# Kernel tuning notes

Hardware: AMD Instinct MI355X
Metric: run time of the kernel (lower is better)

The kernel has to match this reference:

```python
import jax, jax.numpy as jnp
import numpy as np
from jax import lax

N = 100000      # nodes
E = 1600000     # edges
T = 8           # timesteps
DS, DT = 10, 20 # static / temporal features
GH = 64         # gnn_hidden
LH = 64         # lstm_hidden
EC = 64         # end_channels
OC = 1          # out_channels
EPS = 1e-5


def setup_inputs() -> dict:
    key = jax.random.key(0)
    ks = jax.random.split(key, 20)
    g = lambda i, shape, s=0.05: jax.random.normal(ks[i], shape, jnp.float32) * s
    return {
        "x": jax.random.normal(ks[0], (N, DS + DT, T), jnp.float32),
        "edge_index": jax.random.randint(ks[1], (2, E), 0, N, jnp.int64),
        # static encoder (computed in forward but unused downstream, kept for faithfulness)
        "W_static": g(2, (GH, DS)), "b_static": g(3, (GH,)),
        # LSTMCell: input_size = DT + GH, hidden = LH; gate order i,f,g,o
        "W_ih": g(4, (4 * LH, DT + GH)), "W_hh": g(5, (4 * LH, LH)),
        "b_ih": g(6, (4 * LH,)), "b_hh": g(7, (4 * LH,)),
        # GraphConv(lstm_hidden -> gnn_hidden): lin_rel (with bias) on aggregated msgs + lin_root (no bias)
        "W_rel": g(8, (GH, LH)), "b_rel": g(9, (GH,)), "W_root": g(10, (GH, LH)),
        # BatchNorm1d(GH+LH)
        "gamma": jnp.ones((GH + LH,), jnp.float32), "beta": jnp.zeros((GH + LH,), jnp.float32),
        # head: linear1(128->EC), linear2(EC->128), output_layer(128->OC)
        "W1": g(11, (EC, GH + LH)), "b1": g(12, (EC,)),
        "W2": g(13, (GH + LH, EC)), "b2": g(14, (GH + LH,)),
        "W_out": g(15, (OC, GH + LH)), "b_out": g(16, (OC,)),
    }


def reference(x, edge_index, W_static, b_static, W_ih, W_hh, b_ih, b_hh,
              W_rel, b_rel, W_root, gamma, beta, W1, b1, W2, b2, W_out, b_out):
    src, dst = edge_index[0], edge_index[1]
    x_static = x[:, :DS, 0]                      # [N, DS]
    x_temporal = x[:, DS:DS + DT, :]             # [N, DT, T]
    static_embed = x_static @ W_static.T + b_static  # computed but unused (matches source)

    xt_seq = jnp.transpose(x_temporal, (2, 0, 1))  # [T, N, DT]
    h0 = jnp.zeros((N, GH), jnp.float32)
    c0 = jnp.zeros((N, GH), jnp.float32)

    def step(carry, x_t):
        h, c = carry
        # GraphConv: sum-aggregate neighbor h, then linear (linear commutes with sum)
        agg = jax.ops.segment_sum(h[src], dst, num_segments=N)   # [N, LH]
        gnn_out = agg @ W_rel.T + b_rel + h @ W_root.T           # [N, GH]
        inp = jnp.concatenate([x_t, gnn_out], axis=1)            # [N, DT+GH]
        gates = inp @ W_ih.T + b_ih + h @ W_hh.T + b_hh          # [N, 4*LH]
        i, f, g_, o = jnp.split(gates, 4, axis=1)
        c_new = jax.nn.sigmoid(f) * c + jax.nn.sigmoid(i) * jnp.tanh(g_)
        h_new = jax.nn.sigmoid(o) * jnp.tanh(c_new)
        return (h_new, c_new), gnn_out

    (h, c), gnn_outs = lax.scan(step, (h0, c0), xt_seq)
    gnn_out = gnn_outs[-1]  # gnn output computed at the last timestep (pre-update h)

    fused = jnp.concatenate([h, gnn_out], axis=1)                # [N, GH+LH]
    # BatchNorm1d, training-mode batch statistics (dropout p set to 0)
    mean = fused.mean(axis=0)
    var = fused.var(axis=0)
    normed = (fused - mean) * lax.rsqrt(var + EPS) * gamma + beta
    h1 = jax.nn.relu(normed @ W1.T + b1)
    hidden = jax.nn.relu(h1 @ W2.T + b2)
    out = jax.nn.sigmoid(hidden @ W_out.T + b_out)               # binary task -> sigmoid
    return out
```

## Files before the change

### kernel.cpp

```cpp
#include <hip/hip_runtime.h>

#define NN 100000
#define NE 1600000
#define TT 8
#define KF 160
#define XSTR 24
#define HISTB 6250
#define NRANGE 8
#define RSPAN 12500

typedef __attribute__((ext_vector_type(8))) short bf16x8;
typedef __attribute__((ext_vector_type(4))) float f32x4;
typedef unsigned int uint_;
typedef unsigned short ushort_;

__device__ __forceinline__ float sigf(float x) { return 1.f / (1.f + __expf(-x)); }
__device__ __forceinline__ float tanhf_(float x) { return 1.f - 2.f / (__expf(2.f * x) + 1.f); }
__device__ __forceinline__ ushort_ f2b(float f) {
    uint_ u = __float_as_uint(f);
    u += 0x7fff + ((u >> 16) & 1);
    return (ushort_)(u >> 16);
}
__device__ __forceinline__ float bl(uint_ u) { return __uint_as_float(u << 16); }
__device__ __forceinline__ float bh(uint_ u) { return __uint_as_float(u & 0xffff0000u); }
__device__ __forceinline__ void acc8(float* a, uint4 v) {
    a[0] += bl(v.x); a[1] += bh(v.x); a[2] += bl(v.y); a[3] += bh(v.y);
    a[4] += bl(v.z); a[5] += bh(v.z); a[6] += bl(v.w); a[7] += bh(v.w);
}
__device__ __forceinline__ uint_ pk(float a, float b) {
    return (uint_)f2b(a) | ((uint_)f2b(b) << 16);
}

__global__ void k_detect(const int* __restrict__ ei, int* flag) {
    int i = blockIdx.x * 256 + threadIdx.x;
    if (ei[2 * i + 1] != 0) atomicOr(flag, 1);
}

__global__ void k_hist_xt(const int* __restrict__ ei, const int* __restrict__ flag, int* cnt,
                          const float* __restrict__ x, ushort_* __restrict__ xT) {
    int b = blockIdx.x;
    if (b < HISTB) {
        int e = b * 256 + threadIdx.x;
        if (e >= NE) return;
        int is32 = *flag;
        int d = is32 ? ei[NE + e] : ei[2 * (NE + e)];
        atomicAdd(&cnt[d], 1);
    } else {
        if (!xT) return;
        int i = (b - HISTB) * 256 + threadIdx.x;
        if (i >= NN * XSTR) return;
        int n = i / XSTR, kk = i - n * XSTR;
        if (kk < 20) {
            const float* xp = x + (size_t)n * 240 + (10 + kk) * 8;
#pragma unroll
            for (int t = 0; t < 8; t++) xT[(size_t)t * NN * XSTR + i] = f2b(xp[t]);
        } else {
#pragma unroll
            for (int t = 0; t < 8; t++) xT[(size_t)t * NN * XSTR + i] = 0;
        }
    }
}

__global__ void k_scanblk(const int* __restrict__ cnt, int* off, int* bsum) {
    __shared__ int tmp[1024];
    int i = blockIdx.x * 1024 + threadIdx.x;
    int v = (i < NN) ? cnt[i] : 0;
    tmp[threadIdx.x] = v;
    __syncthreads();
    for (int d = 1; d < 1024; d <<= 1) {
        int t = (threadIdx.x >= d) ? tmp[threadIdx.x - d] : 0;
        __syncthreads();
        tmp[threadIdx.x] += t;
        __syncthreads();
    }
    if (i < NN) off[i + 1] = tmp[threadIdx.x];
    if (threadIdx.x == 1023) bsum[blockIdx.x] = tmp[1023];
}

__global__ void k_scantop(int* bsum, int nb) {
    if (threadIdx.x == 0) {
        int run = 0;
        for (int b = 0; b < nb; b++) { int t = bsum[b]; bsum[b] = run; run += t; }
    }
}

__global__ void k_scanadd(int* off, const int* __restrict__ bsum) {
    int i = blockIdx.x * 1024 + threadIdx.x;
    if (i < NN) off[i + 1] += bsum[blockIdx.x];
    if (i == 0) off[0] = 0;
}

__global__ void k_scatter(const int* __restrict__ ei, const int* __restrict__ flag,
                          int* cursor, int* csr) {
    int b = blockIdx.x;
    int range = b & (NRANGE - 1), chunk = b >> 3;
    int e = chunk * 256 + threadIdx.x;
    if (e >= NE) return;
    int is32 = *flag;
    int d = is32 ? ei[NE + e] : ei[2 * (NE + e)];
    if (d / RSPAN != range) return;
    int s = is32 ? ei[e] : ei[2 * e];
    int pos = atomicAdd(&cursor[d], 1);
    csr[pos] = s;
}

__global__ void k_prep(const float* __restrict__ W_ih, const float* __restrict__ W_hh,
                       const float* __restrict__ b_ih, const float* __restrict__ b_hh,
                       const float* __restrict__ W_rel, const float* __restrict__ b_rel,
                       const float* __restrict__ W_root, ushort_* WgB, float* bgp) {
    int n = threadIdx.x;
    int k = blockIdx.x;
    if (k < KF) {
        float v = 0.f;
        if (n < 256) {
            int w = n >> 6, g = (n >> 4) & 3, j = w * 16 + (n & 15);
            int row = g * 64 + j;
            if (k < 20) {
                v = W_ih[row * 84 + k];
            } else if (k >= 24 && k < 88) {
                int kk = k - 24;
                float a = 0.f;
                for (int m = 0; m < 64; m++) a += W_ih[row * 84 + 20 + m] * W_rel[m * 64 + kk];
                v = a;
            } else if (k >= 88 && k < 152) {
                int kk = k - 88;
                float a = W_hh[row * 64 + kk];
                for (int m = 0; m < 64; m++) a += W_ih[row * 84 + 20 + m] * W_root[m * 64 + kk];
                v = a;
            }
        } else {
            int j = n - 256;
            if (k >= 24 && k < 88) v = W_rel[j * 64 + (k - 24)];
            else if (k >= 88 && k < 152) v = W_root[j * 64 + (k - 88)];
        }
        WgB[(size_t)n * KF + k] = f2b(v);
    } else {
        if (n < 256) {
            int j = n >> 2, g = n & 3;
            int row = g * 64 + j;
            float a = b_ih[row] + b_hh[row];
            for (int m = 0; m < 64; m++) a += W_ih[row * 84 + 20 + m] * b_rel[m];
            bgp[n] = a;
        } else {
            bgp[n] = b_rel[n - 256];
        }
    }
}

template <bool LAST>
__device__ __forceinline__ void step_body(const float* __restrict__ x,
                                          const ushort_* __restrict__ xT,
                                          const int* __restrict__ off,
                                          const int* __restrict__ csr,
                                          const ushort_* __restrict__ hbR,
                                          ushort_* __restrict__ hbW,
                                          float* __restrict__ hf,
                                          float* __restrict__ c,
                                          const ushort_* __restrict__ WgB,
                                          const float* __restrict__ bgp,
                                          float* __restrict__ gnn,
                                          float* __restrict__ sums,
                                          float* __restrict__ sumsq, int t) {
    constexpr int NT = LAST ? 5 : 4;
    __shared__ __align__(16) ushort_ Zs[64 * 168];
    const int tid = threadIdx.x;
    const int nblk = blockIdx.x * 64;
    const int w = tid >> 6, lane = tid & 63;
    const int q = lane >> 4, l16 = lane & 15;

#pragma unroll
    for (int i = 0; i < 3; ++i) {
        int slot = tid + 256 * i;
        int n = slot / 12, oo = slot - n * 12;
        int n_g = nblk + n;
        uint4 z = make_uint4(0, 0, 0, 0);
        if (n_g < NN) {
            if (oo < 3) {
                if (xT) {
                    z = *(const uint4*)(xT + ((size_t)t * NN + n_g) * XSTR + oo * 8);
                } else {
                    const float* xp = x + (size_t)n_g * 240 + 80 + (size_t)oo * 64 + t;
                    uint_ r[4];
#pragma unroll
                    for (int p = 0; p < 4; p++) {
                        int k0 = oo * 8 + p * 2;
                        ushort_ b0 = (k0 < 20) ? f2b(xp[p * 16]) : (ushort_)0;
                        ushort_ b1 = (k0 + 1 < 20) ? f2b(xp[p * 16 + 8]) : (ushort_)0;
                        r[p] = (uint_)b0 | ((uint_)b1 << 16);
                    }
                    z = make_uint4(r[0], r[1], r[2], r[3]);
                }
            } else if (oo < 11) {
                z = *(const uint4*)(hbR + (size_t)n_g * 64 + (oo - 3) * 8);
            }
        }
        int oct = (oo < 3) ? oo : ((oo < 11) ? (oo + 8) : 19);
        *(uint4*)(Zs + n * 168 + oct * 8) = z;
    }

    {
        int slot = tid >> 3;
        int l8 = tid & 7;
        for (int nn = slot; nn < 64; nn += 32) {
            int node = nblk + nn;
            float a[8];
#pragma unroll
            for (int i = 0; i < 8; i++) a[i] = 0.f;
            if (t > 0 && node < NN) {
                int e0 = off[node], e1 = off[node + 1];
                int e = e0;
                for (; e + 8 <= e1; e += 8) {
                    uint4 v0 = *(const uint4*)(hbR + (size_t)csr[e] * 64 + l8 * 8);
                    uint4 v1 = *(const uint4*)(hbR + (size_t)csr[e + 1] * 64 + l8 * 8);
                    uint4 v2 = *(const uint4*)(hbR + (size_t)csr[e + 2] * 64 + l8 * 8);
                    uint4 v3 = *(const uint4*)(hbR + (size_t)csr[e + 3] * 64 + l8 * 8);
                    uint4 v4 = *(const uint4*)(hbR + (size_t)csr[e + 4] * 64 + l8 * 8);
                    uint4 v5 = *(const uint4*)(hbR + (size_t)csr[e + 5] * 64 + l8 * 8);
                    uint4 v6 = *(const uint4*)(hbR + (size_t)csr[e + 6] * 64 + l8 * 8);
                    uint4 v7 = *(const uint4*)(hbR + (size_t)csr[e + 7] * 64 + l8 * 8);
                    acc8(a, v0); acc8(a, v1); acc8(a, v2); acc8(a, v3);
                    acc8(a, v4); acc8(a, v5); acc8(a, v6); acc8(a, v7);
                }
                for (; e < e1; e++) {
                    uint4 v0 = *(const uint4*)(hbR + (size_t)csr[e] * 64 + l8 * 8);
                    acc8(a, v0);
                }
            }
            uint4 o;
            o.x = pk(a[0], a[1]); o.y = pk(a[2], a[3]);
            o.z = pk(a[4], a[5]); o.w = pk(a[6], a[7]);
            *(uint4*)(Zs + nn * 168 + 24 + l8 * 8) = o;
        }
    }
    __syncthreads();

    f32x4 acc[4][NT];
#pragma unroll
    for (int mt = 0; mt < 4; mt++)
#pragma unroll
        for (int nt = 0; nt < NT; nt++) acc[mt][nt] = (f32x4)(0.f);

#pragma unroll
    for (int kt = 0; kt < 5; ++kt) {
        bf16x8 af[4], bf[NT];
#pragma unroll
        for (int mt = 0; mt < 4; mt++)
            af[mt] = *(const bf16x8*)(Zs + (mt * 16 + l16) * 168 + kt * 32 + q * 8);
#pragma unroll
        for (int nt = 0; nt < NT; nt++) {
            int n = (nt < 4) ? (w * 64 + nt * 16 + l16) : (256 + w * 16 + l16);
            bf[nt] = *(const bf16x8*)(WgB + (size_t)n * KF + kt * 32 + q * 8);
        }
#pragma unroll
        for (int mt = 0; mt < 4; mt++)
#pragma unroll
            for (int nt = 0; nt < NT; nt++)
                acc[mt][nt] = __builtin_amdgcn_mfma_f32_16x16x32_bf16(af[mt], bf[nt], acc[mt][nt], 0, 0, 0);
    }

    const int j = w * 16 + l16;
    const f32x4 bias = *(const f32x4*)(bgp + j * 4);
    const float brl = LAST ? bgp[256 + j] : 0.f;
    float sh = 0.f, sh2 = 0.f, sg = 0.f, sg2 = 0.f;

    __syncthreads();
    ushort_* Hs   = Zs;
    float*   CsLo = (float*)(Zs + 4096);

    float cnHi[8];
#pragma unroll
    for (int mt = 0; mt < 4; ++mt) {
#pragma unroll
        for (int r = 0; r < 4; ++r) {
            int nloc = mt * 16 + q * 4 + r;
            int node = nblk + nloc;
            float cn = 0.f, hn = 0.f;
            if (node < NN) {
                size_t idx = (size_t)node * 64 + j;
                float iv = sigf(acc[mt][0][r] + bias.x);
                float fv = sigf(acc[mt][1][r] + bias.y);
                float gv = tanhf_(acc[mt][2][r] + bias.z);
                float ov = sigf(acc[mt][3][r] + bias.w);
                cn = fv * c[idx] + iv * gv;
                hn = ov * tanhf_(cn);
                if (LAST) {
                    float gn = acc[mt][4][r] + brl;
                    hf[idx] = hn;
                    gnn[idx] = gn;
                    sh += hn; sh2 += hn * hn;
                    sg += gn; sg2 += gn * gn;
                }
            }
            Hs[nloc * 64 + j] = f2b(hn);
            if (mt < 2) CsLo[nloc * 64 + j] = cn;
            else        cnHi[(mt - 2) * 4 + r] = cn;
        }
    }
    __syncthreads();
#pragma unroll
    for (int i = 0; i < 2; ++i) {
        int s = tid + 256 * i;
        {
            int n = s >> 3, part = s & 7;
            if (nblk + n < NN)
                *(uint4*)(hbW + (size_t)(nblk + n) * 64 + part * 8) =
                    *(const uint4*)(Hs + n * 64 + part * 8);
        }
        {
            int n = s >> 4, part = s & 15;
            if (nblk + n < NN)
                *(float4*)(c + (size_t)(nblk + n) * 64 + part * 4) =
                    *(const float4*)(CsLo + n * 64 + part * 4);
        }
    }
    __syncthreads();
    float* CsHi = (float*)Zs;
#pragma unroll
    for (int mt = 2; mt < 4; ++mt)
#pragma unroll
        for (int r = 0; r < 4; ++r) {
            int nloc = mt * 16 + q * 4 + r;
            CsHi[(nloc - 32) * 64 + j] = cnHi[(mt - 2) * 4 + r];
        }
    __syncthreads();
#pragma unroll
    for (int i = 0; i < 2; ++i) {
        int s = tid + 256 * i;
        int n = 32 + (s >> 4), part = s & 15;
        if (nblk + n < NN)
            *(float4*)(c + (size_t)(nblk + n) * 64 + part * 4) =
                *(const float4*)(CsHi + (n - 32) * 64 + part * 4);
    }

    if (LAST) {
#pragma unroll
        for (int d = 16; d < 64; d <<= 1) {
            sh += __shfl_xor(sh, d, 64);
            sh2 += __shfl_xor(sh2, d, 64);
            sg += __shfl_xor(sg, d, 64);
            sg2 += __shfl_xor(sg2, d, 64);
        }
        if (q == 0) {
            atomicAdd(&sums[j], sh);
            atomicAdd(&sumsq[j], sh2);
            atomicAdd(&sums[64 + j], sg);
            atomicAdd(&sumsq[64 + j], sg2);
        }
    }
}

__global__ __launch_bounds__(256, 4) void k_step(const float* __restrict__ x,
                                                 const ushort_* __restrict__ xT,
                                                 const int* __restrict__ off,
                                                 const int* __restrict__ csr,
                                                 const ushort_* __restrict__ hbR,
                                                 ushort_* __restrict__ hbW,
                                                 float* __restrict__ hf,
                                                 float* __restrict__ c,
                                                 const ushort_* __restrict__ WgB,
                                                 const float* __restrict__ bgp, int t) {
    step_body<false>(x, xT, off, csr, hbR, hbW, hf, c, WgB, bgp, nullptr, nullptr, nullptr, t);
}

__global__ __launch_bounds__(256, 4) void k_stepL(const float* __restrict__ x,
                                                  const ushort_* __restrict__ xT,
                                                  const int* __restrict__ off,
                                                  const int* __restrict__ csr,
                                                  const ushort_* __restrict__ hbR,
                                                  ushort_* __restrict__ hbW,
                                                  float* __restrict__ hf,
                                                  float* __restrict__ c,
                                                  const ushort_* __restrict__ WgB,
                                                  const float* __restrict__ bgp,
                                                  float* __restrict__ gnn,
                                                  float* __restrict__ sums,
                                                  float* __restrict__ sumsq, int t) {
    step_body<true>(x, xT, off, csr, hbR, hbW, hf, c, WgB, bgp, gnn, sums, sumsq, t);
}

__global__ __launch_bounds__(256) void k_head(const float* __restrict__ hf,
                                              const float* __restrict__ gnn,
                                              const float* __restrict__ sums,
                                              const float* __restrict__ sumsq,
                                              const float* __restrict__ gamma,
                                              const float* __restrict__ beta,
                                              const float* __restrict__ W1,
                                              const float* __restrict__ b1,
                                              const float* __restrict__ W2,
                                              const float* __restrict__ b2,
                                              const float* __restrict__ W_out,
                                              const float* __restrict__ b_out,
                                              float* __restrict__ out) {
    __shared__ __align__(16) ushort_ Zs[64 * 168];
    __shared__ __align__(16) ushort_ W1s[64 * 168];
    __shared__ __align__(16) ushort_ W2s[128 * 72];
    __shared__ __align__(16) ushort_ H1s[64 * 72];
    __shared__ float ab[256];
    __shared__ float Obuf[4][64];
    const int tid = threadIdx.x;
    const int w = tid >> 6, lane = tid & 63;
    const int q = lane >> 4, l16 = lane & 15;

    if (tid < 128) {
        float mean = sums[tid] / (float)NN;
        float var = sumsq[tid] / (float)NN - mean * mean;
        float a = gamma[tid] * rsqrtf(var + 1e-5f);
        ab[tid] = a;
        ab[128 + tid] = beta[tid] - mean * a;
    }
#pragma unroll
    for (int i = 0; i < 8; ++i) {
        int slot = tid + 256 * i;
        int jj = slot >> 5, k4 = slot & 31;
        float4 v = *(const float4*)(W1 + (size_t)jj * 128 + k4 * 4);
        *(uint2*)(W1s + jj * 168 + k4 * 4) = make_uint2(pk(v.x, v.y), pk(v.z, v.w));
    }
#pragma unroll
    for (int i = 0; i < 8; ++i) {
        int slot = tid + 256 * i;
        int jj = slot >> 4, k4 = slot & 15;
        float4 v = *(const float4*)(W2 + (size_t)jj * 64 + k4 * 4);
        *(uint2*)(W2s + jj * 72 + k4 * 4) = make_uint2(pk(v.x, v.y), pk(v.z, v.w));
    }
    const int j1 = w * 16 + l16;
    const float bb1 = b1[j1];
    const int j2a = (w * 2) * 16 + l16, j2b = (w * 2 + 1) * 16 + l16;
    const float bb2a = b2[j2a], bb2b = b2[j2b];
    const float woa = W_out[j2a], wob = W_out[j2b];
    const float bo = b_out[0];
    __syncthreads();

    const int NTILE = (NN + 63) / 64;
    for (int tile = blockIdx.x; tile < NTILE; tile += gridDim.x) {
        const int nblk = tile * 64;
#pragma unroll
        for (int i = 0; i < 8; ++i) {
            int slot = tid + 256 * i;
            int n = slot >> 5, f4 = slot & 31;
            int n_g = nblk + n;
            uint2 z = make_uint2(0, 0);
            if (n_g < NN) {
                const float* src = (f4 < 16) ? (hf + (size_t)n_g * 64 + f4 * 4)
                                             : (gnn + (size_t)n_g * 64 + (f4 - 16) * 4);
                float4 v = *(const float4*)src;
                int F = f4 * 4;
                z = make_uint2(pk(v.x * ab[F] + ab[128 + F], v.y * ab[F + 1] + ab[129 + F]),
                               pk(v.z * ab[F + 2] + ab[130 + F], v.w * ab[F + 3] + ab[131 + F]));
            }
            *(uint2*)(Zs + n * 168 + f4 * 4) = z;
        }
        __syncthreads();
        f32x4 acc1[4];
#pragma unroll
        for (int mt = 0; mt < 4; mt++) acc1[mt] = (f32x4)(0.f);
#pragma unroll
        for (int kt = 0; kt < 4; ++kt) {
            bf16x8 bfw = *(const bf16x8*)(W1s + j1 * 168 + kt * 32 + q * 8);
#pragma unroll
            for (int mt = 0; mt < 4; mt++) {
                bf16x8 af = *(const bf16x8*)(Zs + (mt * 16 + l16) * 168 + kt * 32 + q * 8);
                acc1[mt] = __builtin_amdgcn_mfma_f32_16x16x32_bf16(af, bfw, acc1[mt], 0, 0, 0);
            }
        }
#pragma unroll
        for (int mt = 0; mt < 4; mt++)
#pragma unroll
            for (int r = 0; r < 4; r++) {
                int nloc = mt * 16 + q * 4 + r;
                H1s[nloc * 72 + j1] = f2b(fmaxf(acc1[mt][r] + bb1, 0.f));
            }
        __syncthreads();
        f32x4 acc2[4][2];
#pragma unroll
        for (int mt = 0; mt < 4; mt++)
#pragma unroll
            for (int nt = 0; nt < 2; nt++) acc2[mt][nt] = (f32x4)(0.f);
#pragma unroll
        for (int kt = 0; kt < 2; ++kt) {
            bf16x8 bfa = *(const bf16x8*)(W2s + j2a * 72 + kt * 32 + q * 8);
            bf16x8 bfb = *(const bf16x8*)(W2s + j2b * 72 + kt * 32 + q * 8);
#pragma unroll
            for (int mt = 0; mt < 4; mt++) {
                bf16x8 af = *(const bf16x8*)(H1s + (mt * 16 + l16) * 72 + kt * 32 + q * 8);
                acc2[mt][0] = __builtin_amdgcn_mfma_f32_16x16x32_bf16(af, bfa, acc2[mt][0], 0, 0, 0);
                acc2[mt][1] = __builtin_amdgcn_mfma_f32_16x16x32_bf16(af, bfb, acc2[mt][1], 0, 0, 0);
            }
        }
#pragma unroll
        for (int mt = 0; mt < 4; mt++) {
#pragma unroll
            for (int r = 0; r < 4; r++) {
                float p = fmaxf(acc2[mt][0][r] + bb2a, 0.f) * woa +
                          fmaxf(acc2[mt][1][r] + bb2b, 0.f) * wob;
#pragma unroll
                for (int d = 1; d < 16; d <<= 1) p += __shfl_xor(p, d, 64);
                if (l16 == 0) Obuf[w][mt * 16 + q * 4 + r] = p;
            }
        }
        __syncthreads();
        if (tid < 64) {
            int n_g = nblk + tid;
            if (n_g < NN) {
                float s = Obuf[0][tid] + Obuf[1][tid] + Obuf[2][tid] + Obuf[3][tid];
                out[n_g] = sigf(s + bo);
            }
        }
        __syncthreads();
    }
}

extern "C" void kernel_launch(void* const* d_in, const int* in_sizes, int n_in,
                              void* d_out, int out_size, void* d_ws, size_t ws_size,
                              hipStream_t stream) {
    const float* x      = (const float*)d_in[0];
    const int*   ei     = (const int*)d_in[1];
    const float* W_ih   = (const float*)d_in[4];
    const float* W_hh   = (const float*)d_in[5];
    const float* b_ih   = (const float*)d_in[6];
    const float* b_hh   = (const float*)d_in[7];
    const float* W_rel  = (const float*)d_in[8];
    const float* b_rel  = (const float*)d_in[9];
    const float* W_root = (const float*)d_in[10];
    const float* gamma  = (const float*)d_in[11];
    const float* beta   = (const float*)d_in[12];
    const float* W1     = (const float*)d_in[13];
    const float* b1     = (const float*)d_in[14];
    const float* W2     = (const float*)d_in[15];
    const float* b2     = (const float*)d_in[16];
    const float* W_out  = (const float*)d_in[17];
    const float* b_out  = (const float*)d_in[18];
    float* out = (float*)d_out;

    char* ws = (char*)d_ws;
    size_t o = 0;
    auto carve = [&](size_t bytes) { char* p = ws + o; o += (bytes + 255) & ~(size_t)255; return p; };
    int*     off   = (int*)carve((NN + 1) * 4);
    int*     cnt   = (int*)carve(NN * 4);
    int*     bsum  = (int*)carve(128 * 4);
    int*     flag  = (int*)carve(256);
    int*     csr   = (int*)carve((size_t)NE * 4);
    float*   hf    = (float*)carve((size_t)NN * 64 * 4);
    float*   c     = (float*)carve((size_t)NN * 64 * 4);
    float*   gnn   = (float*)carve((size_t)NN * 64 * 4);
    ushort_* hbA   = (ushort_*)carve((size_t)NN * 64 * 2);
    ushort_* hbB   = (ushort_*)carve((size_t)NN * 64 * 2);
    ushort_* WgB   = (ushort_*)carve((size_t)320 * KF * 2);
    float*   bgp   = (float*)carve(320 * 4);
    float*   sums  = (float*)carve(128 * 4);
    float*   sumsq = (float*)carve(128 * 4);
    ushort_* xT = nullptr;
    size_t need_xt = (size_t)TT * NN * XSTR * 2;
    if (o + need_xt + 256 <= ws_size) xT = (ushort_*)carve(need_xt);

    const int nscan = (NN + 1023) / 1024;
    const int xtb = xT ? (NN * XSTR + 255) / 256 : 0;

    hipMemsetAsync(flag, 0, 4, stream);
    hipMemsetAsync(cnt, 0, NN * 4, stream);
    k_detect<<<16, 256, 0, stream>>>(ei, flag);
    k_hist_xt<<<HISTB + xtb, 256, 0, stream>>>(ei, flag, cnt, x, xT);
    k_scanblk<<<nscan, 1024, 0, stream>>>(cnt, off, bsum);
    k_scantop<<<1, 64, 0, stream>>>(bsum, nscan);
    k_scanadd<<<nscan, 1024, 0, stream>>>(off, bsum);
    hipMemcpyAsync(cnt, off, NN * 4, hipMemcpyDeviceToDevice, stream);
    k_scatter<<<(NE / 256) * NRANGE, 256, 0, stream>>>(ei, flag, cnt, csr);

    hipMemsetAsync(c, 0, (size_t)NN * 64 * 4, stream);
    hipMemsetAsync(hbA, 0, (size_t)NN * 64 * 2, stream);
    hipMemsetAsync(sums, 0, 1024, stream);
    k_prep<<<KF + 1, 320, 0, stream>>>(W_ih, W_hh, b_ih, b_hh, W_rel, b_rel, W_root, WgB, bgp);

    const int ngates = (NN + 63) / 64;
    for (int t = 0; t < TT; ++t) {
        ushort_* hbR = (t & 1) ? hbB : hbA;
        ushort_* hbW = (t & 1) ? hbA : hbB;
        if (t == TT - 1)
            k_stepL<<<ngates, 256, 0, stream>>>(x, xT, off, csr, hbR, hbW, hf, c,
                                                WgB, bgp, gnn, sums, sumsq, t);
        else
            k_step<<<ngates, 256, 0, stream>>>(x, xT, off, csr, hbR, hbW, hf, c,
                                               WgB, bgp, t);
    }

    k_head<<<512, 256, 0, stream>>>(hf, gnn, sums, sumsq, gamma, beta,
                                    W1, b1, W2, b2, W_out, b_out, out);
}
```

Before: 920.5 us.

## Skip zero-state memsets, software-pipeline gather, split last-step GNN GEMM, nontemporal loads

Drops the memsets of c and the first h buffer and instead treats t==0 state as zero in-kernel. Adds nontemporal loads for the per-step x slice and the old cell state. Rotates the neighbor-gather loop so eight loads are in flight while the previous batch accumulates. In the last step, computes the GNN-output MFMA tile separately before the gate MFMAs to lower register pressure. The aim is less memory traffic and more latency hiding in the per-step kernel, at the cost of more code paths.

```diff
diff --git a/kernel.cpp b/kernel.cpp
--- a/kernel.cpp
+++ b/kernel.cpp
@@ -13,6 +13,7 @@
 typedef __attribute__((ext_vector_type(4))) float f32x4;
 typedef unsigned int uint_;
 typedef unsigned short ushort_;
+typedef __attribute__((ext_vector_type(4))) uint_ u32x4;
 
 __device__ __forceinline__ float sigf(float x) { return 1.f / (1.f + __expf(-x)); }
 __device__ __forceinline__ float tanhf_(float x) { return 1.f - 2.f / (__expf(2.f * x) + 1.f); }
@@ -29,6 +30,10 @@
 }
 __device__ __forceinline__ uint_ pk(float a, float b) {
     return (uint_)f2b(a) | ((uint_)f2b(b) << 16);
+}
+__device__ __forceinline__ uint4 ntld16(const void* p) {
+    u32x4 v = __builtin_nontemporal_load((const u32x4*)p);
+    return make_uint4(v[0], v[1], v[2], v[3]);
 }
 
 __global__ void k_detect(const int* __restrict__ ei, int* flag) {
@@ -161,7 +166,6 @@
                                           float* __restrict__ gnn,
                                           float* __restrict__ sums,
                                           float* __restrict__ sumsq, int t) {
-    constexpr int NT = LAST ? 5 : 4;
     __shared__ __align__(16) ushort_ Zs[64 * 168];
     const int tid = threadIdx.x;
     const int nblk = blockIdx.x * 64;
@@ -177,7 +181,7 @@
         if (n_g < NN) {
             if (oo < 3) {
                 if (xT) {
-                    z = *(const uint4*)(xT + ((size_t)t * NN + n_g) * XSTR + oo * 8);
+                    z = ntld16(xT + ((size_t)t * NN + n_g) * XSTR + oo * 8);
                 } else {
                     const float* xp = x + (size_t)n_g * 240 + 80 + (size_t)oo * 64 + t;
                     uint_ r[4];
@@ -191,7 +195,8 @@
                     z = make_uint4(r[0], r[1], r[2], r[3]);
                 }
             } else if (oo < 11) {
-                z = *(const uint4*)(hbR + (size_t)n_g * 64 + (oo - 3) * 8);
+                if (t > 0)
+                    z = *(const uint4*)(hbR + (size_t)n_g * 64 + (oo - 3) * 8);
             }
         }
         int oct = (oo < 3) ? oo : ((oo < 11) ? (oo + 8) : 19);
@@ -209,17 +214,26 @@
             if (t > 0 && node < NN) {
                 int e0 = off[node], e1 = off[node + 1];
                 int e = e0;
-                for (; e + 8 <= e1; e += 8) {
-                    uint4 v0 = *(const uint4*)(hbR + (size_t)csr[e] * 64 + l8 * 8);
-                    uint4 v1 = *(const uint4*)(hbR + (size_t)csr[e + 1] * 64 + l8 * 8);
-                    uint4 v2 = *(const uint4*)(hbR + (size_t)csr[e + 2] * 64 + l8 * 8);
-                    uint4 v3 = *(const uint4*)(hbR + (size_t)csr[e + 3] * 64 + l8 * 8);
-                    uint4 v4 = *(const uint4*)(hbR + (size_t)csr[e + 4] * 64 + l8 * 8);
-                    uint4 v5 = *(const uint4*)(hbR + (size_t)csr[e + 5] * 64 + l8 * 8);
-                    uint4 v6 = *(const uint4*)(hbR + (size_t)csr[e + 6] * 64 + l8 * 8);
-                    uint4 v7 = *(const uint4*)(hbR + (size_t)csr[e + 7] * 64 + l8 * 8);
-                    acc8(a, v0); acc8(a, v1); acc8(a, v2); acc8(a, v3);
-                    acc8(a, v4); acc8(a, v5); acc8(a, v6); acc8(a, v7);
+                if (e + 8 <= e1) {
+                    uint4 v[8];
+#pragma unroll
+                    for (int i = 0; i < 8; i++)
+                        v[i] = *(const uint4*)(hbR + (size_t)csr[e + i] * 64 + l8 * 8);
+                    e += 8;
+                    for (; e + 8 <= e1; e += 8) {
+#pragma unroll
+                        for (int i = 0; i < 4; i++) {
+                            acc8(a, v[i]);
+                            v[i] = *(const uint4*)(hbR + (size_t)csr[e + i] * 64 + l8 * 8);
+                        }
+#pragma unroll
+                        for (int i = 4; i < 8; i++) {
+                            acc8(a, v[i]);
+                            v[i] = *(const uint4*)(hbR + (size_t)csr[e + i] * 64 + l8 * 8);
+                        }
+                    }
+#pragma unroll
+                    for (int i = 0; i < 8; i++) acc8(a, v[i]);
                 }
                 for (; e < e1; e++) {
                     uint4 v0 = *(const uint4*)(hbR + (size_t)csr[e] * 64 + l8 * 8);
@@ -234,34 +248,61 @@
     }
     __syncthreads();
 
-    f32x4 acc[4][NT];
+    const int j = w * 16 + l16;
+    float sh = 0.f, sh2 = 0.f, sg = 0.f, sg2 = 0.f;
+
+    if (LAST) {
+        f32x4 accg[4];
+#pragma unroll
+        for (int mt = 0; mt < 4; mt++) accg[mt] = (f32x4)(0.f);
+#pragma unroll
+        for (int kt = 0; kt < 5; ++kt) {
+            bf16x8 bfg = *(const bf16x8*)(WgB + (size_t)(256 + w * 16 + l16) * KF + kt * 32 + q * 8);
+#pragma unroll
+            for (int mt = 0; mt < 4; mt++) {
+                bf16x8 af = *(const bf16x8*)(Zs + (mt * 16 + l16) * 168 + kt * 32 + q * 8);
+                accg[mt] = __builtin_amdgcn_mfma_f32_16x16x32_bf16(af, bfg, accg[mt], 0, 0, 0);
+            }
+        }
+        const float brl = bgp[256 + j];
+#pragma unroll
+        for (int mt = 0; mt < 4; ++mt)
+#pragma unroll
+            for (int r = 0; r < 4; ++r) {
+                int node = nblk + mt * 16 + q * 4 + r;
+                if (node < NN) {
+                    float gn = accg[mt][r] + brl;
+                    gnn[(size_t)node * 64 + j] = gn;
+                    sg += gn; sg2 += gn * gn;
+                }
+            }
+    }
+
+    f32x4 acc[4][4];
 #pragma unroll
     for (int mt = 0; mt < 4; mt++)
 #pragma unroll
-        for (int nt = 0; nt < NT; nt++) acc[mt][nt] = (f32x4)(0.f);
+        for (int nt = 0; nt < 4; nt++) acc[mt][nt] = (f32x4)(0.f);
 
 #pragma unroll
     for (int kt = 0; kt < 5; ++kt) {
-        bf16x8 af[4], bf[NT];
+        bf16x8 af[4], bf[4];
 #pragma unroll
         for (int mt = 0; mt < 4; mt++)
             af[mt] = *(const bf16x8*)(Zs + (mt * 16 + l16) * 168 + kt * 32 + q * 8);
 #pragma unroll
-        for (int nt = 0; nt < NT; nt++) {
-            int n = (nt < 4) ? (w * 64 + nt * 16 + l16) : (256 + w * 16 + l16);
+        for (int nt = 0; nt < 4; nt++) {
+            int n = w * 64 + nt * 16 + l16;
             bf[nt] = *(const bf16x8*)(WgB + (size_t)n * KF + kt * 32 + q * 8);
         }
 #pragma unroll
         for (int mt = 0; mt < 4; mt++)
 #pragma unroll
-            for (int nt = 0; nt < NT; nt++)
+            for (int nt = 0; nt < 4; nt++)
                 acc[mt][nt] = __builtin_amdgcn_mfma_f32_16x16x32_bf16(af[mt], bf[nt], acc[mt][nt], 0, 0, 0);
     }
 
-    const int j = w * 16 + l16;
     const f32x4 bias = *(const f32x4*)(bgp + j * 4);
-    const float brl = LAST ? bgp[256 + j] : 0.f;
-    float sh = 0.f, sh2 = 0.f, sg = 0.f, sg2 = 0.f;
 
     __syncthreads();
     ushort_* Hs   = Zs;
@@ -281,14 +322,13 @@
                 float fv = sigf(acc[mt][1][r] + bias.y);
                 float gv = tanhf_(acc[mt][2][r] + bias.z);
                 float ov = sigf(acc[mt][3][r] + bias.w);
-                cn = fv * c[idx] + iv * gv;
+                float cold = 0.f;
+                if (t > 0) cold = __builtin_nontemporal_load(c + idx);
+                cn = fv * cold + iv * gv;
                 hn = ov * tanhf_(cn);
                 if (LAST) {
-                    float gn = acc[mt][4][r] + brl;
                     hf[idx] = hn;
-                    gnn[idx] = gn;
                     sh += hn; sh2 += hn * hn;
-                    sg += gn; sg2 += gn * gn;
                 }
             }
             Hs[nloc * 64 + j] = f2b(hn);
@@ -565,8 +605,6 @@
     hipMemcpyAsync(cnt, off, NN * 4, hipMemcpyDeviceToDevice, stream);
     k_scatter<<<(NE / 256) * NRANGE, 256, 0, stream>>>(ei, flag, cnt, csr);
 
-    hipMemsetAsync(c, 0, (size_t)NN * 64 * 4, stream);
-    hipMemsetAsync(hbA, 0, (size_t)NN * 64 * 2, stream);
     hipMemsetAsync(sums, 0, 1024, stream);
     k_prep<<<KF + 1, 320, 0, stream>>>(W_ih, W_hh, b_ih, b_hh, W_rel, b_rel, W_root, WgB, bgp);
 
```

Result: slower. 942.2 us (+2.4%).
